# Kernel tuning notes

Measured on AMD Instinct MI355X. Metric: run time of the kernel, lower is better.

Reference implementation:

```python
import jax, jax.numpy as jnp
import numpy as np
import math

B, W, D_IN, H = 64, 512, 300, 512

def setup_inputs() -> dict:
    key = jax.random.key(0)
    ks = jax.random.split(key, 8)
    s = 1.0 / math.sqrt(D_IN)
    return {
        "char_vectors": jax.random.normal(ks[0], (B, W, D_IN), jnp.float32),
        "word_vectors": jax.random.normal(ks[1], (B, W, D_IN), jnp.float32),
        "Wk": jax.random.uniform(ks[2], (D_IN, H), jnp.float32, -s, s),
        "bk": jnp.zeros((H,), jnp.float32),
        "Wq": jax.random.uniform(ks[3], (D_IN, H), jnp.float32, -s, s),
        "bq": jnp.zeros((H,), jnp.float32),
        "Wv": jax.random.uniform(ks[4], (D_IN, H), jnp.float32, -s, s),
        "bv": jnp.zeros((H,), jnp.float32),
    }

def reference(char_vectors, word_vectors, Wk, bk, Wq, bq, Wv, bv):
    # Stack word/char reps per word -> [B, W, 2, H]
    def proj(Wm, bm):
        return jnp.stack([word_vectors @ Wm + bm, char_vectors @ Wm + bm], axis=2)
    K = proj(Wk, bk)
    Q = proj(Wq, bq)
    V = proj(Wv, bv)
    temp = jnp.sqrt(jnp.asarray(H, jnp.float32))
    # tiny 2x2 attention per word, fully batched (dropout off = eval mode)
    attn = jnp.einsum("bwqh,bwkh->bwqk", Q, K) / temp
    attn = jax.nn.softmax(attn, axis=-1)
    out = jnp.einsum("bwqk,bwkh->bwqh", attn, V)  # [B, W, 2, H]
    return out.reshape(B, W, 2 * H)
```

## Files before the change

kernel.cpp:

```cpp
#include <hip/hip_runtime.h>

#define D 300
#define HDIM 512
#define ROWS 256
#define WPB 128
#define NKS 20
#define NCH 24
#define CH_BYTES 40960
#define CH_ELEMS 20480
#define REG_BYTES 20480
#define SEGW 5

typedef __attribute__((ext_vector_type(16))) float f32x16;
typedef __attribute__((ext_vector_type(4))) float f32x4;
typedef __attribute__((ext_vector_type(8))) short bf16x8;

__device__ inline unsigned short f2bf(float f) {
  unsigned int u = __float_as_uint(f);
  unsigned int r = (u + 0x7fffu + ((u >> 16) & 1u)) >> 16;
  return (unsigned short)r;
}

__device__ inline void gload_lds16(const void* g, void* l) {
  __builtin_amdgcn_global_load_lds(
      (const __attribute__((address_space(1))) unsigned int*)g,
      (__attribute__((address_space(3))) unsigned int*)l, 16, 0, 0);
}

__global__ __launch_bounds__(512) void prep_weights(
    const float* __restrict__ Wq, const float* __restrict__ Wk,
    const float* __restrict__ Wv, const float* __restrict__ bq,
    const float* __restrict__ bk, const float* __restrict__ bv,
    unsigned short* __restrict__ wt) {
  int idx = blockIdx.x * 512 + threadIdx.x;
  if (idx >= NCH * CH_ELEMS) return;
  int c = idx / CH_ELEMS, r = idx - c * CH_ELEMS;
  int reg = r / 10240, r2 = r - reg * 10240;
  int ks = r2 >> 9, r3 = r2 & 511;
  int kh = r3 >> 8, r4 = r3 & 255;
  int col = r4 >> 3, e = r4 & 7;
  int k = ks * 16 + kh * 8 + e;
  const float* M; const float* B; int gcol;
  if (c < 16) {
    M = reg ? Wk : Wq; B = reg ? bk : bq; gcol = c * 32 + col;
  } else {
    M = Wv; B = bv; gcol = (c - 16) * 64 + reg * 32 + col;
  }
  float v = (k < D) ? M[k * HDIM + gcol] : ((k == D) ? B[gcol] : 0.0f);
  wt[idx] = f2bf(v);
}

__global__ __launch_bounds__(512) void fused_attn(
    const float* __restrict__ charv, const float* __restrict__ wordv,
    const unsigned short* __restrict__ wt, float* __restrict__ out) {
  extern __shared__ char lds[];
  float* sS  = (float*)(lds + 3 * CH_BYTES);
  float* sAt = sS;

  const int tid  = threadIdx.x;
  const int wid  = tid >> 6;
  const int lane = tid & 63;
  const int lo5  = lane & 31;
  const int hi   = lane >> 5;

  auto stage = [&](int t) {
    const char* src = (const char*)wt + (long)t * CH_BYTES + wid * (SEGW * 1024) + lane * 16;
    char* dst = lds + (t % 3) * CH_BYTES + wid * (SEGW * 1024);
#pragma unroll
    for (int j = 0; j < SEGW; ++j)
      gload_lds16(src + j * 1024, dst + j * 1024);
  };

  stage(0);
  stage(1);

  bf16x8 a[NKS];
  {
    int row = blockIdx.x * ROWS + wid * 32 + lo5;
    const float* rp = ((row & 1) ? charv : wordv) + (row >> 1) * D;
#pragma unroll
    for (int ks = 0; ks < NKS; ++ks) {
      int k0 = ks * 16 + hi * 8;
      float4 lo = {0.f, 0.f, 0.f, 0.f}, hif = {0.f, 0.f, 0.f, 0.f};
      if (k0 + 8 <= D) {
        lo  = *(const float4*)(rp + k0);
        hif = *(const float4*)(rp + k0 + 4);
      } else if (k0 < D) {
        lo  = *(const float4*)(rp + k0);
      }
      bf16x8 v;
      v[0] = (short)f2bf(lo.x);  v[1] = (short)f2bf(lo.y);
      v[2] = (short)f2bf(lo.z);  v[3] = (short)f2bf(lo.w);
      v[4] = (short)f2bf(hif.x); v[5] = (short)f2bf(hif.y);
      v[6] = (short)f2bf(hif.z); v[7] = (short)f2bf(hif.w);
      if (ks == 18 && hi == 1) v[4] = (short)0x3F80;
      a[ks] = v;
    }
  }

  float p[32];
#pragma unroll
  for (int t = 0; t < 32; ++t) p[t] = 0.f;

  for (int t = 0; t < 16; ++t) {
    asm volatile("s_waitcnt vmcnt(5)" ::: "memory");
    asm volatile("s_waitcnt lgkmcnt(0)" ::: "memory");
    __builtin_amdgcn_s_barrier();
    stage(t + 2);
    const char* base = lds + (t % 3) * CH_BYTES + hi * 512 + lo5 * 16;
    f32x16 accQ, accK;
#pragma unroll
    for (int r = 0; r < 16; ++r) { accQ[r] = 0.f; accK[r] = 0.f; }
    __builtin_amdgcn_s_setprio(1);
#pragma unroll
    for (int ks = 0; ks < NKS; ++ks) {
      bf16x8 qb = *(const bf16x8*)(base + ks * 1024);
      bf16x8 kb = *(const bf16x8*)(base + REG_BYTES + ks * 1024);
      accQ = __builtin_amdgcn_mfma_f32_32x32x16_bf16(a[ks], qb, accQ, 0, 0, 0);
      accK = __builtin_amdgcn_mfma_f32_32x32x16_bf16(a[ks], kb, accK, 0, 0, 0);
    }
    __builtin_amdgcn_s_setprio(0);
#pragma unroll
    for (int tt = 0; tt < 8; ++tt)
#pragma unroll
      for (int i = 0; i < 2; ++i)
#pragma unroll
        for (int j = 0; j < 2; ++j)
          p[tt * 4 + i * 2 + j] += accQ[2 * tt + i] * accK[2 * tt + j];
  }

#pragma unroll
  for (int t = 0; t < 32; ++t) {
    float v = p[t];
    v += __shfl_xor(v, 1);
    v += __shfl_xor(v, 2);
    v += __shfl_xor(v, 4);
    v += __shfl_xor(v, 8);
    v += __shfl_xor(v, 16);
    p[t] = v;
  }
  if (lo5 == 0) {
#pragma unroll
    for (int tt = 0; tt < 8; ++tt) {
      int w = wid * 16 + (tt >> 1) * 4 + (tt & 1) + hi * 2;
#pragma unroll
      for (int q = 0; q < 4; ++q) sS[w * 4 + q] = p[tt * 4 + q];
    }
  }
  asm volatile("s_waitcnt lgkmcnt(0)" ::: "memory");
  __builtin_amdgcn_s_barrier();
  if (tid < 128) {
    const float sc = 0.044194173824159216f;
    float s[4];
#pragma unroll
    for (int t = 0; t < 4; ++t) s[t] = sS[tid * 4 + t] * sc;
#pragma unroll
    for (int i = 0; i < 2; ++i) {
      float m  = fmaxf(s[i * 2], s[i * 2 + 1]);
      float e0 = expf(s[i * 2] - m), e1 = expf(s[i * 2 + 1] - m);
      float inv = 1.0f / (e0 + e1);
      sAt[tid * 4 + i * 2]     = e0 * inv;
      sAt[tid * 4 + i * 2 + 1] = e1 * inv;
    }
  }
  asm volatile("s_waitcnt lgkmcnt(0)" ::: "memory");
  __builtin_amdgcn_s_barrier();

  f32x4 at[8];
#pragma unroll
  for (int tt = 0; tt < 8; ++tt) {
    int w = wid * 16 + (tt >> 1) * 4 + (tt & 1) + hi * 2;
    at[tt] = *(const f32x4*)(sAt + w * 4);
  }

  for (int t = 16; t < NCH; ++t) {
    if (t == 16) asm volatile("s_waitcnt vmcnt(5)" ::: "memory");
    else         asm volatile("s_waitcnt vmcnt(37)" ::: "memory");
    asm volatile("s_waitcnt lgkmcnt(0)" ::: "memory");
    __builtin_amdgcn_s_barrier();
    if (t + 2 < NCH) stage(t + 2);
    const char* base = lds + (t % 3) * CH_BYTES + hi * 512 + lo5 * 16;
    const int g = t - 16;
#pragma unroll
    for (int ct = 0; ct < 2; ++ct) {
      f32x16 accV;
#pragma unroll
      for (int r = 0; r < 16; ++r) accV[r] = 0.f;
      __builtin_amdgcn_s_setprio(1);
#pragma unroll
      for (int ks = 0; ks < NKS; ++ks) {
        bf16x8 vb = *(const bf16x8*)(base + ct * REG_BYTES + ks * 1024);
        accV = __builtin_amdgcn_mfma_f32_32x32x16_bf16(a[ks], vb, accV, 0, 0, 0);
      }
      __builtin_amdgcn_s_setprio(0);
      int h = g * 64 + ct * 32 + lo5;
#pragma unroll
      for (int tt = 0; tt < 8; ++tt) {
        int w = wid * 16 + (tt >> 1) * 4 + (tt & 1) + hi * 2;
        long gw = (long)(blockIdx.x * WPB + w);
        float v0 = accV[2 * tt], v1 = accV[2 * tt + 1];
        out[gw * 1024 + h]       = at[tt][0] * v0 + at[tt][1] * v1;
        out[gw * 1024 + 512 + h] = at[tt][2] * v0 + at[tt][3] * v1;
      }
    }
  }
}

extern "C" void kernel_launch(void* const* d_in, const int* in_sizes, int n_in,
                              void* d_out, int out_size, void* d_ws, size_t ws_size,
                              hipStream_t stream) {
  const float* charv = (const float*)d_in[0];
  const float* wordv = (const float*)d_in[1];
  const float* Wk = (const float*)d_in[2];
  const float* bk = (const float*)d_in[3];
  const float* Wq = (const float*)d_in[4];
  const float* bq = (const float*)d_in[5];
  const float* Wv = (const float*)d_in[6];
  const float* bv = (const float*)d_in[7];
  float* out = (float*)d_out;
  unsigned short* wt = (unsigned short*)d_ws;

  prep_weights<<<(NCH * CH_ELEMS + 511) / 512, 512, 0, stream>>>(
      Wq, Wk, Wv, bq, bk, bv, wt);

  const int lds_bytes = 3 * CH_BYTES + 512 * 4;
  fused_attn<<<65536 / ROWS, 512, lds_bytes, stream>>>(charv, wordv, wt, out);
}
```

Baseline: 87.96 us.

## Precompute Wq·Wk^T to replace Q/K projections with one bilinear form

The per-word scores Q·K^T are rewritten as x·(Wq Wk^T)·y, where the bias is folded in as an augmented row and column. A prep kernel builds the 301x301 product matrix. The main kernel then computes x·M with MFMA and extracts the matching input slice with an identity-matrix MFMA, instead of projecting Q and K separately to 512 dims. This cuts the score-phase chunks from 16 to 5 and the K-steps from 20 to 19, at the cost of a heavier prep kernel (a 512-long dot product per element) and extra identity MFMAs.

```diff
diff --git a/kernel.cpp b/kernel.cpp
--- a/kernel.cpp
+++ b/kernel.cpp
@@ -4,11 +4,11 @@
 #define HDIM 512
 #define ROWS 256
 #define WPB 128
-#define NKS 20
-#define NCH 24
-#define CH_BYTES 40960
-#define CH_ELEMS 20480
-#define REG_BYTES 20480
+#define NKS 19
+#define NCH 13
+#define CH_STRIDE 40960
+#define CH_SELEMS 20480
+#define REGB 19456
 #define SEGW 5
 
 typedef __attribute__((ext_vector_type(16))) float f32x16;
@@ -27,34 +27,47 @@
       (__attribute__((address_space(3))) unsigned int*)l, 16, 0, 0);
 }
 
-__global__ __launch_bounds__(512) void prep_weights(
+__global__ __launch_bounds__(256) void prep_weights(
     const float* __restrict__ Wq, const float* __restrict__ Wk,
     const float* __restrict__ Wv, const float* __restrict__ bq,
     const float* __restrict__ bk, const float* __restrict__ bv,
     unsigned short* __restrict__ wt) {
-  int idx = blockIdx.x * 512 + threadIdx.x;
-  if (idx >= NCH * CH_ELEMS) return;
-  int c = idx / CH_ELEMS, r = idx - c * CH_ELEMS;
-  int reg = r / 10240, r2 = r - reg * 10240;
+  int idx = blockIdx.x * 256 + threadIdx.x;
+  if (idx >= NCH * 19456) return;
+  int c = idx / 19456, r = idx - c * 19456;
+  int reg = r / 9728, r2 = r - reg * 9728;
   int ks = r2 >> 9, r3 = r2 & 511;
   int kh = r3 >> 8, r4 = r3 & 255;
   int col = r4 >> 3, e = r4 & 7;
-  int k = ks * 16 + kh * 8 + e;
-  const float* M; const float* B; int gcol;
-  if (c < 16) {
-    M = reg ? Wk : Wq; B = reg ? bk : bq; gcol = c * 32 + col;
+  int k1 = ks * 16 + kh * 8 + e;
+  int addr = c * CH_SELEMS + reg * 9728 + ks * 512 + kh * 256 + col * 8 + e;
+  float v = 0.0f;
+  if (c < 5) {
+    int k2 = c * 64 + reg * 32 + col;
+    if (k1 <= 300 && k2 <= 300) {
+      const float* qrow = (k1 < 300) ? (Wq + k1 * HDIM) : bq;
+      const float* krow = (k2 < 300) ? (Wk + k2 * HDIM) : bk;
+      float acc = 0.f;
+      for (int h = 0; h < HDIM; h += 4) {
+        float4 q4 = *(const float4*)(qrow + h);
+        float4 k4 = *(const float4*)(krow + h);
+        acc += q4.x * k4.x + q4.y * k4.y + q4.z * k4.z + q4.w * k4.w;
+      }
+      v = acc;
+    }
   } else {
-    M = Wv; B = bv; gcol = (c - 16) * 64 + reg * 32 + col;
-  }
-  float v = (k < D) ? M[k * HDIM + gcol] : ((k == D) ? B[gcol] : 0.0f);
-  wt[idx] = f2bf(v);
+    int gcol = (c - 5) * 64 + reg * 32 + col;
+    if (k1 < D)       v = Wv[k1 * HDIM + gcol];
+    else if (k1 == D) v = bv[gcol];
+  }
+  wt[addr] = f2bf(v);
 }
 
 __global__ __launch_bounds__(512) void fused_attn(
     const float* __restrict__ charv, const float* __restrict__ wordv,
     const unsigned short* __restrict__ wt, float* __restrict__ out) {
   extern __shared__ char lds[];
-  float* sS  = (float*)(lds + 3 * CH_BYTES);
+  float* sS  = (float*)(lds + 3 * CH_STRIDE);
   float* sAt = sS;
 
   const int tid  = threadIdx.x;
@@ -64,8 +77,8 @@
   const int hi   = lane >> 5;
 
   auto stage = [&](int t) {
-    const char* src = (const char*)wt + (long)t * CH_BYTES + wid * (SEGW * 1024) + lane * 16;
-    char* dst = lds + (t % 3) * CH_BYTES + wid * (SEGW * 1024);
+    const char* src = (const char*)wt + (long)t * CH_STRIDE + wid * (SEGW * 1024) + lane * 16;
+    char* dst = lds + (t % 3) * CH_STRIDE + wid * (SEGW * 1024);
 #pragma unroll
     for (int j = 0; j < SEGW; ++j)
       gload_lds16(src + j * 1024, dst + j * 1024);
@@ -98,35 +111,50 @@
     }
   }
 
+  bf16x8 i0, i1;
+#pragma unroll
+  for (int e = 0; e < 8; ++e) {
+    i0[e] = (lo5 == hi * 8 + e)      ? (short)0x3F80 : (short)0;
+    i1[e] = (lo5 == 16 + hi * 8 + e) ? (short)0x3F80 : (short)0;
+  }
+
   float p[32];
 #pragma unroll
   for (int t = 0; t < 32; ++t) p[t] = 0.f;
 
-  for (int t = 0; t < 16; ++t) {
+  const f32x16 zero16 = {0.f, 0.f, 0.f, 0.f, 0.f, 0.f, 0.f, 0.f,
+                         0.f, 0.f, 0.f, 0.f, 0.f, 0.f, 0.f, 0.f};
+
+#pragma unroll
+  for (int t = 0; t < 5; ++t) {
     asm volatile("s_waitcnt vmcnt(5)" ::: "memory");
     asm volatile("s_waitcnt lgkmcnt(0)" ::: "memory");
     __builtin_amdgcn_s_barrier();
     stage(t + 2);
-    const char* base = lds + (t % 3) * CH_BYTES + hi * 512 + lo5 * 16;
-    f32x16 accQ, accK;
-#pragma unroll
-    for (int r = 0; r < 16; ++r) { accQ[r] = 0.f; accK[r] = 0.f; }
-    __builtin_amdgcn_s_setprio(1);
-#pragma unroll
-    for (int ks = 0; ks < NKS; ++ks) {
-      bf16x8 qb = *(const bf16x8*)(base + ks * 1024);
-      bf16x8 kb = *(const bf16x8*)(base + REG_BYTES + ks * 1024);
-      accQ = __builtin_amdgcn_mfma_f32_32x32x16_bf16(a[ks], qb, accQ, 0, 0, 0);
-      accK = __builtin_amdgcn_mfma_f32_32x32x16_bf16(a[ks], kb, accK, 0, 0, 0);
-    }
-    __builtin_amdgcn_s_setprio(0);
-#pragma unroll
-    for (int tt = 0; tt < 8; ++tt)
-#pragma unroll
-      for (int i = 0; i < 2; ++i)
-#pragma unroll
-        for (int j = 0; j < 2; ++j)
-          p[tt * 4 + i * 2 + j] += accQ[2 * tt + i] * accK[2 * tt + j];
+    const char* cb = lds + (t % 3) * CH_STRIDE;
+#pragma unroll
+    for (int r = 0; r < 2; ++r) {
+      const char* base = cb + r * REGB + hi * 512 + lo5 * 16;
+      f32x16 accY = zero16;
+      __builtin_amdgcn_s_setprio(1);
+#pragma unroll
+      for (int ks = 0; ks < NKS; ++ks) {
+        bf16x8 mb = *(const bf16x8*)(base + ks * 1024);
+        accY = __builtin_amdgcn_mfma_f32_32x32x16_bf16(a[ks], mb, accY, 0, 0, 0);
+      }
+      const int ks0 = t * 4 + r * 2;
+      f32x16 accX = __builtin_amdgcn_mfma_f32_32x32x16_bf16(a[ks0], i0, zero16, 0, 0, 0);
+      if (ks0 + 1 < NKS)
+        accX = __builtin_amdgcn_mfma_f32_32x32x16_bf16(a[ks0 + 1], i1, accX, 0, 0, 0);
+      __builtin_amdgcn_s_setprio(0);
+#pragma unroll
+      for (int tt = 0; tt < 8; ++tt)
+#pragma unroll
+        for (int i = 0; i < 2; ++i)
+#pragma unroll
+          for (int j = 0; j < 2; ++j)
+            p[tt * 4 + i * 2 + j] += accY[2 * tt + i] * accX[2 * tt + j];
+    }
   }
 
 #pragma unroll
@@ -173,23 +201,21 @@
     at[tt] = *(const f32x4*)(sAt + w * 4);
   }
 
-  for (int t = 16; t < NCH; ++t) {
-    if (t == 16) asm volatile("s_waitcnt vmcnt(5)" ::: "memory");
-    else         asm volatile("s_waitcnt vmcnt(37)" ::: "memory");
+  for (int t = 5; t < NCH; ++t) {
+    if (t == 5) asm volatile("s_waitcnt vmcnt(5)" ::: "memory");
+    else        asm volatile("s_waitcnt vmcnt(37)" ::: "memory");
     asm volatile("s_waitcnt lgkmcnt(0)" ::: "memory");
     __builtin_amdgcn_s_barrier();
     if (t + 2 < NCH) stage(t + 2);
-    const char* base = lds + (t % 3) * CH_BYTES + hi * 512 + lo5 * 16;
-    const int g = t - 16;
+    const char* base = lds + (t % 3) * CH_STRIDE + hi * 512 + lo5 * 16;
+    const int g = t - 5;
 #pragma unroll
     for (int ct = 0; ct < 2; ++ct) {
-      f32x16 accV;
-#pragma unroll
-      for (int r = 0; r < 16; ++r) accV[r] = 0.f;
+      f32x16 accV = zero16;
       __builtin_amdgcn_s_setprio(1);
 #pragma unroll
       for (int ks = 0; ks < NKS; ++ks) {
-        bf16x8 vb = *(const bf16x8*)(base + ct * REG_BYTES + ks * 1024);
+        bf16x8 vb = *(const bf16x8*)(base + ct * REGB + ks * 1024);
         accV = __builtin_amdgcn_mfma_f32_32x32x16_bf16(a[ks], vb, accV, 0, 0, 0);
       }
       __builtin_amdgcn_s_setprio(0);
@@ -220,9 +246,9 @@
   float* out = (float*)d_out;
   unsigned short* wt = (unsigned short*)d_ws;
 
-  prep_weights<<<(NCH * CH_ELEMS + 511) / 512, 512, 0, stream>>>(
+  prep_weights<<<(NCH * 19456 + 255) / 256, 256, 0, stream>>>(
       Wq, Wk, Wv, bq, bk, bv, wt);
 
-  const int lds_bytes = 3 * CH_BYTES + 512 * 4;
+  const int lds_bytes = 3 * CH_STRIDE + 512 * 4;
   fused_attn<<<65536 / ROWS, 512, lds_bytes, stream>>>(charv, wordv, wt, out);
 }
```

New measurement: 112.3 us. 1.28x slower.
